# Kernel tuning notes

Hardware: AMD Instinct MI355X
Metric: run time of the kernel (lower is better)

The kernel has to match this reference:

```python
import jax, jax.numpy as jnp
import numpy as np
from jax import lax

HEADS = 8
DIM_HEAD = 64
SCALE = DIM_HEAD ** -0.5

def conv2d(x, w, stride=1, pad=0):
    return lax.conv_general_dilated(
        x, w, window_strides=(stride, stride),
        padding=[(pad, pad), (pad, pad)],
        dimension_numbers=("NCHW", "OIHW", "NCHW"))

def setup_inputs() -> dict:
    key = jax.random.key(0)
    ks = jax.random.split(key, 5)
    b, dim, H, W = 8, 256, 32, 32
    inner = HEADS * DIM_HEAD  # 512
    x = jax.random.normal(ks[0], (b, dim, H, W), jnp.float32)
    Wq = jax.random.normal(ks[1], (inner, dim, 1, 1), jnp.float32) * 0.05
    Wkv = jax.random.normal(ks[2], (2 * inner, dim, 3, 3), jnp.float32) * 0.05
    Wout = jax.random.normal(ks[3], (dim, inner, 1, 1), jnp.float32) * 0.05
    bout = jnp.zeros((dim,), jnp.float32)
    return {"x": x, "Wq": Wq, "Wkv": Wkv, "Wout": Wout, "bout": bout}

def reference(x, Wq, Wkv, Wout, bout):
    b = x.shape[0]
    h, d = HEADS, DIM_HEAD
    q = conv2d(x, Wq, stride=1, pad=0)        # [b, h*d, H, W]
    kv = conv2d(x, Wkv, stride=1, pad=1)      # [b, 2*h*d, H, W]
    k, v = jnp.split(kv, 2, axis=1)
    out_h, out_w = q.shape[-2:]

    def to_bhnd(t):
        # b (h d) x y -> b h (x y) d
        B, _, X, Y = t.shape
        return t.reshape(B, h, d, X * Y).transpose(0, 1, 3, 2)

    q, k, v = map(to_bhnd, (q, k, v))
    dots = jnp.einsum("bhid,bhjd->bhij", q, k) * SCALE
    attn = jax.nn.softmax(dots, axis=-1)
    out = jnp.einsum("bhij,bhjd->bhid", attn, v)  # [b, h, n, d]
    # b h (x y) d -> b (h d) x y
    out = out.transpose(0, 1, 3, 2).reshape(b, h * d, out_h, out_w)
    out = jax.nn.gelu(out, approximate=False)
    out = conv2d(out, Wout, stride=1, pad=0) + bout[None, :, None, None]
    return out
```

## Files before the change

kernel.cpp:

```cpp
#include <hip/hip_runtime.h>
#include <math.h>

#define BATCH 8
#define DIM   256
#define NPIX  1024
#define DHEAD 64
#define INNER 512
#define KVCH  1024
#define PPIX  1156

typedef _Float16 half8 __attribute__((ext_vector_type(8)));
typedef _Float16 half4 __attribute__((ext_vector_type(4)));
typedef float    f32x4 __attribute__((ext_vector_type(4)));
#define MFMA16(a, b, c) __builtin_amdgcn_mfma_f32_16x16x32_f16(a, b, c, 0, 0, 0)

static __device__ __forceinline__ float gelu_f(float v) {
    return 0.5f * v * (1.0f + erff(v * 0.70710678118654752440f));
}

static __device__ __forceinline__ void gload16(const _Float16* g, _Float16* l) {
    __builtin_amdgcn_global_load_lds(
        (const __attribute__((address_space(1))) unsigned int*)g,
        (__attribute__((address_space(3))) unsigned int*)l, 16, 0, 0);
}

__global__ __launch_bounds__(256) void prep_w_kernel(
    const float* __restrict__ Wq, const float* __restrict__ Wkv,
    const float* __restrict__ Wout, _Float16* __restrict__ Aq,
    _Float16* __restrict__ Akv, _Float16* __restrict__ Aout)
{
    const int e = blockIdx.x * 256 + threadIdx.x;
    if (e < 131072) Aq[e] = (_Float16)Wq[e];
    const int e2 = e - 131072;
    if (e2 >= 0 && e2 < 2359296) {
        int oc = e2 / 2304, r = e2 - oc * 2304;
        int s = r >> 8, ic = r & 255;
        Akv[e2] = (_Float16)Wkv[oc * 2304 + ic * 9 + s];
    }
    const int e3 = e - 131072 - 2359296;
    if (e3 >= 0 && e3 < 131072) Aout[e3] = (_Float16)Wout[e3];
}

__global__ __launch_bounds__(256) void transpose_x_kernel(
    const float* __restrict__ x, _Float16* __restrict__ xtp)
{
    __shared__ float ts[64][65];
    const int pt = blockIdx.x * 64, ic0 = blockIdx.y * 64, b = blockIdx.z;
    const int tid = threadIdx.x;
    const float* xb = x + (((size_t)(b * DIM + ic0)) << 10) + pt;
#pragma unroll
    for (int e = tid; e < 4096; e += 256) {
        int i = e >> 6, p = e & 63;
        ts[i][p] = xb[((size_t)i << 10) + p];
    }
    __syncthreads();
#pragma unroll
    for (int e = tid; e < 512; e += 256) {
        int p = e >> 3, ig = e & 7;
        int gp = pt + p, y = gp >> 5, xc = gp & 31;
        half8 v;
#pragma unroll
        for (int u = 0; u < 8; ++u) v[u] = (_Float16)ts[ig * 8 + u][p];
        *(half8*)&xtp[((size_t)b * PPIX + (y + 1) * 34 + xc + 1) * 256 + ic0 + ig * 8] = v;
    }
}

__global__ __launch_bounds__(256) void qkv_gemm_kernel(
    const _Float16* __restrict__ Akv, const _Float16* __restrict__ Aq,
    const _Float16* __restrict__ xtp, _Float16* __restrict__ qt,
    _Float16* __restrict__ ktp, _Float16* __restrict__ vb)
{
    __shared__ _Float16 As[128 * 64];
    __shared__ _Float16 Bs[64 * 64];
    const int nt = blockIdx.x, mt = blockIdx.y, b = blockIdx.z;
    const bool QBLK = (mt >= 8);
    const int tid = threadIdx.x;
    const int w = tid >> 6, lane = tid & 63;
    const int quad = lane >> 4, l15 = lane & 15;
    const int m0 = (QBLK ? mt - 8 : mt) * 128, p0 = nt * 64;
    const int wm = w * 32;
    const f32x4 Z4 = {0.f, 0.f, 0.f, 0.f};

    const int srow = lane >> 3;
    const int scol = ((lane & 7) ^ srow) * 8;

    const _Float16* abase = QBLK ? Aq : Akv;
    const int astride = QBLK ? 256 : 2304;
    const int ktend = QBLK ? 4 : 36;

    const _Float16* agp[4];
#pragma unroll
    for (int c = 0; c < 4; ++c) {
        int row = (w * 4 + c) * 8 + srow;
        agp[c] = abase + (size_t)(m0 + row) * astride + scol;
    }
    const _Float16* bgp[2];
#pragma unroll
    for (int c = 0; c < 2; ++c) {
        int row = (w * 2 + c) * 8 + srow;
        int p = p0 + row, py = p >> 5, px = p & 31;
        bgp[c] = xtp + ((size_t)b * PPIX + (py + 1) * 34 + px + 1) * 256 + scol;
    }

    f32x4 acc[2][4];
#pragma unroll
    for (int mi = 0; mi < 2; ++mi)
#pragma unroll
        for (int ni = 0; ni < 4; ++ni) acc[mi][ni] = Z4;

    for (int kt = 0; kt < ktend; ++kt) {
        __syncthreads();
        const int s = QBLK ? 4 : (kt >> 2);
        const int doff = (s / 3 - 1) * 34 + (s - (s / 3) * 3) - 1;
        const int boff = doff * 256 + (kt & 3) * 64;
#pragma unroll
        for (int c = 0; c < 4; ++c)
            gload16(agp[c] + kt * 64, &As[(w * 4 + c) * 512]);
#pragma unroll
        for (int c = 0; c < 2; ++c)
            gload16(bgp[c] + boff, &Bs[(w * 2 + c) * 512]);
        __syncthreads();
#pragma unroll
        for (int ks = 0; ks < 2; ++ks) {
            half8 av[2], bv[4];
#pragma unroll
            for (int mi = 0; mi < 2; ++mi) {
                const int r = wm + mi * 16 + l15;
                av[mi] = *(const half8*)&As[r * 64 + (((ks * 4 + quad) ^ (l15 & 7)) << 3)];
            }
#pragma unroll
            for (int ni = 0; ni < 4; ++ni) {
                const int r = ni * 16 + l15;
                bv[ni] = *(const half8*)&Bs[r * 64 + (((ks * 4 + quad) ^ (l15 & 7)) << 3)];
            }
#pragma unroll
            for (int mi = 0; mi < 2; ++mi)
#pragma unroll
                for (int ni = 0; ni < 4; ++ni)
                    acc[mi][ni] = MFMA16(av[mi], bv[ni], acc[mi][ni]);
        }
    }

#pragma unroll
    for (int mi = 0; mi < 2; ++mi) {
        const int mbase = m0 + wm + mi * 16;
        if (!QBLK && mbase >= 512) {
#pragma unroll
            for (int r = 0; r < 4; ++r) {
                const int mv = mbase + quad * 4 + r - 512;
#pragma unroll
                for (int ni = 0; ni < 4; ++ni) {
                    const int pix = p0 + ni * 16 + l15;
                    vb[(((size_t)(b * 512 + mv)) << 10) + pix] = (_Float16)acc[mi][ni][r];
                }
            }
        } else {
            const int h  = mbase >> 6;
            const int dd = (mbase & 63) + quad * 4;
            _Float16* dst = QBLK ? qt : ktp;
#pragma unroll
            for (int ni = 0; ni < 4; ++ni) {
                const int pix = p0 + ni * 16 + l15;
                half4 v4;
#pragma unroll
                for (int r = 0; r < 4; ++r) {
                    float vv = acc[mi][ni][r];
                    if (QBLK) vv *= 0.125f;
                    v4[r] = (_Float16)vv;
                }
                *(half4*)&dst[((((size_t)(b * 8 + h)) << 10) + pix) * 64 + dd] = v4;
            }
        }
    }
}

template<int M, int K, int KROW>
__global__ __launch_bounds__(256) void out_gemm_kernel(
    const _Float16* __restrict__ A, const _Float16* __restrict__ act,
    float* __restrict__ Cout, const float* __restrict__ bias)
{
    __shared__ _Float16 As[128 * 64];
    __shared__ _Float16 Bs[64 * 64];
    const int nt = blockIdx.x, mt = blockIdx.y, b = blockIdx.z;
    const int tid = threadIdx.x;
    const int w = tid >> 6, lane = tid & 63;
    const int quad = lane >> 4, l15 = lane & 15;
    const int m0 = mt * 128, p0 = nt * 64;
    const int wm = w * 32;
    const f32x4 Z4 = {0.f, 0.f, 0.f, 0.f};

    const int srow = lane >> 3;
    const int scol = ((lane & 7) ^ srow) * 8;

    const _Float16* agp[4];
#pragma unroll
    for (int c = 0; c < 4; ++c) {
        int row = (w * 4 + c) * 8 + srow;
        agp[c] = A + (size_t)(m0 + row) * K + scol;
    }
    const _Float16* bgp[2];
#pragma unroll
    for (int c = 0; c < 2; ++c) {
        int row = (w * 2 + c) * 8 + srow;
        bgp[c] = act + (size_t)(b * NPIX + p0 + row) * KROW + scol;
    }

    f32x4 acc[2][4];
#pragma unroll
    for (int mi = 0; mi < 2; ++mi)
#pragma unroll
        for (int ni = 0; ni < 4; ++ni) acc[mi][ni] = Z4;

    for (int kt = 0; kt < K / 64; ++kt) {
        __syncthreads();
#pragma unroll
        for (int c = 0; c < 4; ++c)
            gload16(agp[c] + kt * 64, &As[(w * 4 + c) * 512]);
#pragma unroll
        for (int c = 0; c < 2; ++c)
            gload16(bgp[c] + kt * 64, &Bs[(w * 2 + c) * 512]);
        __syncthreads();
#pragma unroll
        for (int ks = 0; ks < 2; ++ks) {
            half8 av[2], bv[4];
#pragma unroll
            for (int mi = 0; mi < 2; ++mi) {
                const int r = wm + mi * 16 + l15;
                av[mi] = *(const half8*)&As[r * 64 + (((ks * 4 + quad) ^ (l15 & 7)) << 3)];
            }
#pragma unroll
            for (int ni = 0; ni < 4; ++ni) {
                const int r = ni * 16 + l15;
                bv[ni] = *(const half8*)&Bs[r * 64 + (((ks * 4 + quad) ^ (l15 & 7)) << 3)];
            }
#pragma unroll
            for (int mi = 0; mi < 2; ++mi)
#pragma unroll
                for (int ni = 0; ni < 4; ++ni)
                    acc[mi][ni] = MFMA16(av[mi], bv[ni], acc[mi][ni]);
        }
    }

#pragma unroll
    for (int mi = 0; mi < 2; ++mi) {
#pragma unroll
        for (int r = 0; r < 4; ++r) {
            const int m = m0 + wm + mi * 16 + quad * 4 + r;
            const float bv = bias[m];
#pragma unroll
            for (int ni = 0; ni < 4; ++ni) {
                const int pix = p0 + ni * 16 + l15;
                Cout[(((size_t)(b * M + m)) << 10) + pix] = acc[mi][ni][r] + bv;
            }
        }
    }
}

__global__ __launch_bounds__(256) void attn_kernel(
    const _Float16* __restrict__ qt,
    const _Float16* __restrict__ ktp,
    const _Float16* __restrict__ vbb,
    _Float16* __restrict__ gout)
{
    __shared__ _Float16 Ks[128 * 64];
    __shared__ _Float16 Vs[64 * 128];
    __shared__ _Float16 Pb[128 * 128];
    const int qtile = blockIdx.x, bh = blockIdx.y;
    const int b = bh >> 3, h = bh & 7;
    const int p0 = qtile * 128;
    const int tid = threadIdx.x;
    const int w = tid >> 6, lane = tid & 63;
    const int quad = lane >> 4, l15 = lane & 15;
    const f32x4 Z4 = {0.f, 0.f, 0.f, 0.f};

    half8 ones;
#pragma unroll
    for (int u = 0; u < 8; ++u) ones[u] = (_Float16)1.0f;

    half8 qf[2][2];
    {
        const _Float16* qrow =
            qt + ((((size_t)(bh)) << 10) + p0 + w * 32 + l15) * 64;
#pragma unroll
        for (int iff = 0; iff < 2; ++iff)
#pragma unroll
            for (int ks = 0; ks < 2; ++ks)
                qf[iff][ks] = *(const half8*)(qrow + iff * 16 * 64 + ks * 32 + quad * 8);
    }

    const _Float16* kbase = ktp + ((size_t)bh << 16);
    const _Float16* vbase = vbb + (((size_t)(b * 512 + h * 64)) << 10);

    f32x4 oacc[4][2];
#pragma unroll
    for (int mf = 0; mf < 4; ++mf)
#pragma unroll
        for (int iff = 0; iff < 2; ++iff) oacc[mf][iff] = Z4;
    f32x4 racc[2] = {Z4, Z4};

    const int kchunk = (lane & 7) ^ (lane >> 3);
    for (int kt = 0; kt < 8; ++kt) {
        const int pk = kt * 128;
        __syncthreads();
        const _Float16* kg = kbase + (size_t)pk * 64;
#pragma unroll
        for (int i = 0; i < 4; ++i) {
            const int t = i * 4 + w;
            gload16(kg + (t * 8 + (lane >> 3)) * 64 + kchunk * 8, &Ks[t * 512]);
        }
#pragma unroll
        for (int i = 0; i < 4; ++i) {
            const int t = i * 4 + w;
            const int vd = t * 4 + (lane >> 4);
            gload16(vbase + ((size_t)vd << 10) + pk + (((lane & 15) ^ (vd & 15)) << 3),
                    &Vs[t * 512]);
        }
        __syncthreads();

#pragma unroll
        for (int g = 0; g < 2; ++g) {
            f32x4 s[4][2];
#pragma unroll
            for (int jf2 = 0; jf2 < 4; ++jf2) {
                const int jr = (g * 4 + jf2) * 16 + l15;
                const half8 ka0 = *(const half8*)&Ks[jr * 64 + ((quad ^ (l15 & 7)) << 3)];
                const half8 ka1 = *(const half8*)&Ks[jr * 64 + (((4 + quad) ^ (l15 & 7)) << 3)];
#pragma unroll
                for (int iff = 0; iff < 2; ++iff) {
                    s[jf2][iff] = MFMA16(ka0, qf[iff][0], Z4);
                    s[jf2][iff] = MFMA16(ka1, qf[iff][1], s[jf2][iff]);
                }
            }
#pragma unroll
            for (int jf2 = 0; jf2 < 4; ++jf2) {
#pragma unroll
                for (int iff = 0; iff < 2; ++iff) {
                    half4 pv4;
#pragma unroll
                    for (int r = 0; r < 4; ++r)
                        pv4[r] = (_Float16)__expf(s[jf2][iff][r] - 8.0f);
                    const int i = w * 32 + iff * 16 + l15;
                    const int c = ((g * 4 + jf2) << 1) + (quad >> 1);
                    *(half4*)&Pb[i * 128 + ((c ^ l15) << 3) + ((quad & 1) << 2)] = pv4;
                }
            }
        }
#pragma unroll
        for (int kc = 0; kc < 4; ++kc) {
            half8 bv[2];
#pragma unroll
            for (int iff = 0; iff < 2; ++iff) {
                const int i = w * 32 + iff * 16 + l15;
                bv[iff] = *(const half8*)&Pb[i * 128 + (((kc * 4 + quad) ^ l15) << 3)];
                racc[iff] = MFMA16(ones, bv[iff], racc[iff]);
            }
#pragma unroll
            for (int mf = 0; mf < 4; ++mf) {
                const int vr = mf * 16 + l15;
                const half8 va = *(const half8*)&Vs[vr * 128 + (((kc * 4 + quad) ^ l15) << 3)];
#pragma unroll
                for (int iff = 0; iff < 2; ++iff)
                    oacc[mf][iff] = MFMA16(va, bv[iff], oacc[mf][iff]);
            }
        }
    }

    float rinv[2];
#pragma unroll
    for (int iff = 0; iff < 2; ++iff) rinv[iff] = 1.f / racc[iff][0];

    __syncthreads();
    _Float16* scr = Pb;
#pragma unroll
    for (int mf = 0; mf < 4; ++mf) {
#pragma unroll
        for (int iff = 0; iff < 2; ++iff) {
            half4 o4;
#pragma unroll
            for (int r = 0; r < 4; ++r)
                o4[r] = (_Float16)gelu_f(oacc[mf][iff][r] * rinv[iff]);
            const int i = w * 32 + iff * 16 + l15;
            *(half4*)&scr[i * 72 + mf * 16 + quad * 4] = o4;
        }
    }
    __syncthreads();
    _Float16* go = gout + ((size_t)(b * NPIX + p0)) * INNER + h * 64;
#pragma unroll
    for (int it = 0; it < 4; ++it) {
        const int e = tid + it * 256;
        const int p = e >> 3, dg = e & 7;
        *(half8*)(go + (size_t)p * INNER + dg * 8) = *(const half8*)&scr[p * 72 + dg * 8];
    }
}

extern "C" void kernel_launch(void* const* d_in, const int* in_sizes, int n_in,
                              void* d_out, int out_size, void* d_ws, size_t ws_size,
                              hipStream_t stream)
{
    const float* x    = (const float*)d_in[0];
    const float* Wq   = (const float*)d_in[1];
    const float* Wkv  = (const float*)d_in[2];
    const float* Wout = (const float*)d_in[3];
    const float* bout = (const float*)d_in[4];
    float* out = (float*)d_out;

    _Float16* xtp  = (_Float16*)d_ws;
    _Float16* Aq   = xtp  + (size_t)BATCH * PPIX * DIM;
    _Float16* Akv  = Aq   + (size_t)INNER * DIM;
    _Float16* Aout = Akv  + (size_t)KVCH * 2304;
    _Float16* qt   = Aout + (size_t)DIM * INNER;
    _Float16* vb   = qt   + (size_t)BATCH * NPIX * INNER;
    _Float16* ktp  = vb   + (size_t)BATCH * NPIX * INNER;
    _Float16* gout = ktp  + (size_t)BATCH * NPIX * INNER;

    (void)hipMemsetAsync(xtp, 0, (size_t)BATCH * PPIX * DIM * sizeof(_Float16), stream);

    prep_w_kernel<<<10240, 256, 0, stream>>>(Wq, Wkv, Wout, Aq, Akv, Aout);
    transpose_x_kernel<<<dim3(16, 4, BATCH), 256, 0, stream>>>(x, xtp);
    qkv_gemm_kernel<<<dim3(16, 12, BATCH), 256, 0, stream>>>(Akv, Aq, xtp, qt, ktp, vb);
    attn_kernel<<<dim3(8, 64), 256, 0, stream>>>(qt, ktp, vb, gout);
    out_gemm_kernel<DIM, 512, 512>
        <<<dim3(16, 2, BATCH), 256, 0, stream>>>(Aout, gout, out, bout);
}
```

Before: 190.2 us.

## Use 128x128 MFMA32 tiles in QKV GEMM and fuse prep kernels

Result: faster. 176.3 us (-7.4%).

```diff
diff --git a/kernel.cpp b/kernel.cpp
--- a/kernel.cpp
+++ b/kernel.cpp
@@ -12,7 +12,9 @@
 typedef _Float16 half8 __attribute__((ext_vector_type(8)));
 typedef _Float16 half4 __attribute__((ext_vector_type(4)));
 typedef float    f32x4 __attribute__((ext_vector_type(4)));
+typedef float    f32x16 __attribute__((ext_vector_type(16)));
 #define MFMA16(a, b, c) __builtin_amdgcn_mfma_f32_16x16x32_f16(a, b, c, 0, 0, 0)
+#define MFMA32(a, b, c) __builtin_amdgcn_mfma_f32_32x32x16_f16(a, b, c, 0, 0, 0)
 
 static __device__ __forceinline__ float gelu_f(float v) {
     return 0.5f * v * (1.0f + erff(v * 0.70710678118654752440f));
@@ -24,44 +26,55 @@
         (__attribute__((address_space(3))) unsigned int*)l, 16, 0, 0);
 }
 
-__global__ __launch_bounds__(256) void prep_w_kernel(
+__global__ __launch_bounds__(256) void prep_kernel(
     const float* __restrict__ Wq, const float* __restrict__ Wkv,
-    const float* __restrict__ Wout, _Float16* __restrict__ Aq,
-    _Float16* __restrict__ Akv, _Float16* __restrict__ Aout)
+    const float* __restrict__ Wout, const float* __restrict__ x,
+    _Float16* __restrict__ Aq, _Float16* __restrict__ Akv,
+    _Float16* __restrict__ Aout, _Float16* __restrict__ xtp)
 {
-    const int e = blockIdx.x * 256 + threadIdx.x;
-    if (e < 131072) Aq[e] = (_Float16)Wq[e];
-    const int e2 = e - 131072;
-    if (e2 >= 0 && e2 < 2359296) {
-        int oc = e2 / 2304, r = e2 - oc * 2304;
-        int s = r >> 8, ic = r & 255;
-        Akv[e2] = (_Float16)Wkv[oc * 2304 + ic * 9 + s];
-    }
-    const int e3 = e - 131072 - 2359296;
-    if (e3 >= 0 && e3 < 131072) Aout[e3] = (_Float16)Wout[e3];
-}
-
-__global__ __launch_bounds__(256) void transpose_x_kernel(
-    const float* __restrict__ x, _Float16* __restrict__ xtp)
-{
-    __shared__ float ts[64][65];
-    const int pt = blockIdx.x * 64, ic0 = blockIdx.y * 64, b = blockIdx.z;
-    const int tid = threadIdx.x;
-    const float* xb = x + (((size_t)(b * DIM + ic0)) << 10) + pt;
-#pragma unroll
-    for (int e = tid; e < 4096; e += 256) {
-        int i = e >> 6, p = e & 63;
-        ts[i][p] = xb[((size_t)i << 10) + p];
-    }
-    __syncthreads();
-#pragma unroll
-    for (int e = tid; e < 512; e += 256) {
-        int p = e >> 3, ig = e & 7;
-        int gp = pt + p, y = gp >> 5, xc = gp & 31;
-        half8 v;
-#pragma unroll
-        for (int u = 0; u < 8; ++u) v[u] = (_Float16)ts[ig * 8 + u][p];
-        *(half8*)&xtp[((size_t)b * PPIX + (y + 1) * 34 + xc + 1) * 256 + ic0 + ig * 8] = v;
+    const int bid = blockIdx.x, tid = threadIdx.x;
+    if (bid < 512) {
+        __shared__ float ts[64][65];
+        const int pt = (bid & 15) * 64, ic0 = ((bid >> 4) & 3) * 64, b = bid >> 6;
+        const float* xb = x + (((size_t)(b * DIM + ic0)) << 10) + pt;
+#pragma unroll
+        for (int e = tid; e < 4096; e += 256) {
+            int i = e >> 6, p = e & 63;
+            ts[i][p] = xb[((size_t)i << 10) + p];
+        }
+        __syncthreads();
+#pragma unroll
+        for (int e = tid; e < 512; e += 256) {
+            int p = e >> 3, ig = e & 7;
+            int gp = pt + p, y = gp >> 5, xc = gp & 31;
+            half8 v;
+#pragma unroll
+            for (int u = 0; u < 8; ++u) v[u] = (_Float16)ts[ig * 8 + u][p];
+            *(half8*)&xtp[((size_t)b * PPIX + (y + 1) * 34 + xc + 1) * 256 + ic0 + ig * 8] = v;
+        }
+    } else if (bid < 10752) {
+        const int e = (bid - 512) * 256 + tid;
+        if (e < 131072) Aq[e] = (_Float16)Wq[e];
+        const int e2 = e - 131072;
+        if (e2 >= 0 && e2 < 2359296) {
+            int oc = e2 / 2304, r = e2 - oc * 2304;
+            int s = r >> 8, ic = r & 255;
+            Akv[e2] = (_Float16)Wkv[oc * 2304 + ic * 9 + s];
+        }
+        const int e3 = e - 131072 - 2359296;
+        if (e3 >= 0 && e3 < 131072) Aout[e3] = (_Float16)Wout[e3];
+    } else {
+        const int he = (bid - 10752) * 256 + tid;
+        if (he < 270336) {
+            int b = he / 33792;
+            int r = he - b * 33792;
+            int hp = r >> 8, ic = r & 255;
+            int row, col;
+            if (hp < 34)      { row = 0;  col = hp; }
+            else if (hp < 68) { row = 33; col = hp - 34; }
+            else { int k2 = hp - 68; row = 1 + (k2 >> 1); col = (k2 & 1) * 33; }
+            xtp[((size_t)b * PPIX + row * 34 + col) * 256 + ic] = (_Float16)0.f;
+        }
     }
 }
 
@@ -71,15 +84,14 @@
     _Float16* __restrict__ ktp, _Float16* __restrict__ vb)
 {
     __shared__ _Float16 As[128 * 64];
-    __shared__ _Float16 Bs[64 * 64];
+    __shared__ _Float16 Bs[128 * 64];
     const int nt = blockIdx.x, mt = blockIdx.y, b = blockIdx.z;
     const bool QBLK = (mt >= 8);
     const int tid = threadIdx.x;
     const int w = tid >> 6, lane = tid & 63;
-    const int quad = lane >> 4, l15 = lane & 15;
-    const int m0 = (QBLK ? mt - 8 : mt) * 128, p0 = nt * 64;
-    const int wm = w * 32;
-    const f32x4 Z4 = {0.f, 0.f, 0.f, 0.f};
+    const int l31 = lane & 31, kh = lane >> 5;
+    const int m0 = (QBLK ? mt - 8 : mt) * 128, p0 = nt * 128;
+    const int wm = (w >> 1) * 64, wn = (w & 1) * 64;
 
     const int srow = lane >> 3;
     const int scol = ((lane & 7) ^ srow) * 8;
@@ -89,24 +101,22 @@
     const int ktend = QBLK ? 4 : 36;
 
     const _Float16* agp[4];
+    const _Float16* bgp[4];
 #pragma unroll
     for (int c = 0; c < 4; ++c) {
         int row = (w * 4 + c) * 8 + srow;
         agp[c] = abase + (size_t)(m0 + row) * astride + scol;
-    }
-    const _Float16* bgp[2];
-#pragma unroll
-    for (int c = 0; c < 2; ++c) {
-        int row = (w * 2 + c) * 8 + srow;
         int p = p0 + row, py = p >> 5, px = p & 31;
         bgp[c] = xtp + ((size_t)b * PPIX + (py + 1) * 34 + px + 1) * 256 + scol;
     }
 
-    f32x4 acc[2][4];
-#pragma unroll
-    for (int mi = 0; mi < 2; ++mi)
-#pragma unroll
-        for (int ni = 0; ni < 4; ++ni) acc[mi][ni] = Z4;
+    f32x16 acc[2][2];
+#pragma unroll
+    for (int mf = 0; mf < 2; ++mf)
+#pragma unroll
+        for (int nf = 0; nf < 2; ++nf)
+#pragma unroll
+            for (int r = 0; r < 16; ++r) acc[mf][nf][r] = 0.f;
 
     for (int kt = 0; kt < ktend; ++kt) {
         __syncthreads();
@@ -117,58 +127,59 @@
         for (int c = 0; c < 4; ++c)
             gload16(agp[c] + kt * 64, &As[(w * 4 + c) * 512]);
 #pragma unroll
-        for (int c = 0; c < 2; ++c)
-            gload16(bgp[c] + boff, &Bs[(w * 2 + c) * 512]);
-        __syncthreads();
-#pragma unroll
-        for (int ks = 0; ks < 2; ++ks) {
-            half8 av[2], bv[4];
-#pragma unroll
-            for (int mi = 0; mi < 2; ++mi) {
-                const int r = wm + mi * 16 + l15;
-                av[mi] = *(const half8*)&As[r * 64 + (((ks * 4 + quad) ^ (l15 & 7)) << 3)];
-            }
-#pragma unroll
-            for (int ni = 0; ni < 4; ++ni) {
-                const int r = ni * 16 + l15;
-                bv[ni] = *(const half8*)&Bs[r * 64 + (((ks * 4 + quad) ^ (l15 & 7)) << 3)];
-            }
-#pragma unroll
-            for (int mi = 0; mi < 2; ++mi)
-#pragma unroll
-                for (int ni = 0; ni < 4; ++ni)
-                    acc[mi][ni] = MFMA16(av[mi], bv[ni], acc[mi][ni]);
-        }
-    }
-
-#pragma unroll
-    for (int mi = 0; mi < 2; ++mi) {
-        const int mbase = m0 + wm + mi * 16;
+        for (int c = 0; c < 4; ++c)
+            gload16(bgp[c] + boff, &Bs[(w * 4 + c) * 512]);
+        __syncthreads();
+#pragma unroll
+        for (int kc = 0; kc < 4; ++kc) {
+            const int cx = ((((kc << 1) | kh) ^ (l31 & 7)) << 3);
+            half8 af[2], bf[2];
+#pragma unroll
+            for (int mf = 0; mf < 2; ++mf)
+                af[mf] = *(const half8*)&As[(wm + mf * 32 + l31) * 64 + cx];
+#pragma unroll
+            for (int nf = 0; nf < 2; ++nf)
+                bf[nf] = *(const half8*)&Bs[(wn + nf * 32 + l31) * 64 + cx];
+#pragma unroll
+            for (int mf = 0; mf < 2; ++mf)
+#pragma unroll
+                for (int nf = 0; nf < 2; ++nf)
+                    acc[mf][nf] = MFMA32(af[mf], bf[nf], acc[mf][nf]);
+        }
+    }
+
+#pragma unroll
+    for (int mf = 0; mf < 2; ++mf) {
+        const int mbase = m0 + wm + mf * 32;
         if (!QBLK && mbase >= 512) {
 #pragma unroll
-            for (int r = 0; r < 4; ++r) {
-                const int mv = mbase + quad * 4 + r - 512;
-#pragma unroll
-                for (int ni = 0; ni < 4; ++ni) {
-                    const int pix = p0 + ni * 16 + l15;
-                    vb[(((size_t)(b * 512 + mv)) << 10) + pix] = (_Float16)acc[mi][ni][r];
+            for (int nf = 0; nf < 2; ++nf) {
+                const int pix = p0 + wn + nf * 32 + l31;
+#pragma unroll
+                for (int reg = 0; reg < 16; ++reg) {
+                    const int mv = mbase - 512 + (reg & 3) + 8 * (reg >> 2) + 4 * kh;
+                    vb[(((size_t)(b * 512 + mv)) << 10) + pix] =
+                        (_Float16)acc[mf][nf][reg];
                 }
             }
         } else {
-            const int h  = mbase >> 6;
-            const int dd = (mbase & 63) + quad * 4;
+            const int h = mbase >> 6;
+            const int dbase = (mbase & 63) + kh * 4;
             _Float16* dst = QBLK ? qt : ktp;
 #pragma unroll
-            for (int ni = 0; ni < 4; ++ni) {
-                const int pix = p0 + ni * 16 + l15;
-                half4 v4;
-#pragma unroll
-                for (int r = 0; r < 4; ++r) {
-                    float vv = acc[mi][ni][r];
-                    if (QBLK) vv *= 0.125f;
-                    v4[r] = (_Float16)vv;
+            for (int nf = 0; nf < 2; ++nf) {
+                const int pix = p0 + wn + nf * 32 + l31;
+#pragma unroll
+                for (int g = 0; g < 4; ++g) {
+                    half4 v4;
+#pragma unroll
+                    for (int r = 0; r < 4; ++r) {
+                        float vv = acc[mf][nf][g * 4 + r];
+                        if (QBLK) vv *= 0.125f;
+                        v4[r] = (_Float16)vv;
+                    }
+                    *(half4*)&dst[((((size_t)(b * 8 + h)) << 10) + pix) * 64 + dbase + g * 8] = v4;
                 }
-                *(half4*)&dst[((((size_t)(b * 8 + h)) << 10) + pix) * 64 + dd] = v4;
             }
         }
     }
@@ -413,11 +424,8 @@
     _Float16* ktp  = vb   + (size_t)BATCH * NPIX * INNER;
     _Float16* gout = ktp  + (size_t)BATCH * NPIX * INNER;
 
-    (void)hipMemsetAsync(xtp, 0, (size_t)BATCH * PPIX * DIM * sizeof(_Float16), stream);
-
-    prep_w_kernel<<<10240, 256, 0, stream>>>(Wq, Wkv, Wout, Aq, Akv, Aout);
-    transpose_x_kernel<<<dim3(16, 4, BATCH), 256, 0, stream>>>(x, xtp);
-    qkv_gemm_kernel<<<dim3(16, 12, BATCH), 256, 0, stream>>>(Akv, Aq, xtp, qt, ktp, vb);
+    prep_kernel<<<11808, 256, 0, stream>>>(Wq, Wkv, Wout, x, Aq, Akv, Aout, xtp);
+    qkv_gemm_kernel<<<dim3(8, 12, BATCH), 256, 0, stream>>>(Akv, Aq, xtp, qt, ktp, vb);
     attn_kernel<<<dim3(8, 64), 256, 0, stream>>>(qt, ktp, vb, gout);
     out_gemm_kernel<DIM, 512, 512>
         <<<dim3(16, 2, BATCH), 256, 0, stream>>>(Aout, gout, out, bout);
```
